# Kernel tuning notes

Hardware: AMD Instinct MI355X
Metric: run time of the kernel (lower is better)

## Reference

```python
import jax, jax.numpy as jnp
import numpy as np

I_DIM, H_DIM, O_DIM = 4, 8, 1


def setup_inputs() -> dict:
    key = jax.random.key(0)
    ks = jax.random.split(key, 7)
    B, T = 8192, 512
    s_ih = 1.0 / np.sqrt(H_DIM)
    x = jax.random.normal(ks[0], (B, T, I_DIM), dtype=jnp.float32)
    # PyTorch LSTM params: gate order i, f, g, o stacked along first axis (4H)
    W_ih = jax.random.uniform(ks[1], (4 * H_DIM, I_DIM), jnp.float32, -s_ih, s_ih)
    W_hh = jax.random.uniform(ks[2], (4 * H_DIM, H_DIM), jnp.float32, -s_ih, s_ih)
    b_ih = jax.random.uniform(ks[3], (4 * H_DIM,), jnp.float32, -s_ih, s_ih)
    b_hh = jax.random.uniform(ks[4], (4 * H_DIM,), jnp.float32, -s_ih, s_ih)
    W_fc = jax.random.uniform(ks[5], (O_DIM, H_DIM), jnp.float32, -s_ih, s_ih)
    b_fc = jax.random.uniform(ks[6], (O_DIM,), jnp.float32, -s_ih, s_ih)
    return {"x": x, "W_ih": W_ih, "W_hh": W_hh, "b_ih": b_ih, "b_hh": b_hh,
            "W_fc": W_fc, "b_fc": b_fc}


def _lstm_last_hidden(x, W_ih, W_hh, b_ih, b_hh):
    B, T, _ = x.shape
    H = W_hh.shape[1]
    # Precompute input projections for all timesteps: [B, T, 4H] -> [T, B, 4H]
    xg = jnp.einsum('bti,gi->btg', x, W_ih) + b_ih + b_hh
    xg = jnp.transpose(xg, (1, 0, 2))
    h0 = jnp.zeros((B, H), x.dtype)
    c0 = jnp.zeros((B, H), x.dtype)

    def step(carry, g_t):
        h, c = carry
        gates = g_t + h @ W_hh.T  # [B, 4H]
        i, f, g, o = jnp.split(gates, 4, axis=-1)
        i = jax.nn.sigmoid(i)
        f = jax.nn.sigmoid(f)
        g = jnp.tanh(g)
        o = jax.nn.sigmoid(o)
        c = f * c + i * g
        h = o * jnp.tanh(c)
        return (h, c), None

    (h_last, _), _ = jax.lax.scan(step, (h0, c0), xg)
    return h_last  # equals out[:, -1, :]


def reference(x, W_ih, W_hh, b_ih, b_hh, W_fc, b_fc):
    h_last = _lstm_last_hidden(x, W_ih, W_hh, b_ih, b_hh)
    return h_last @ W_fc.T + b_fc  # [B, output_dim]
```

## Files before the change

### kernel.cpp

```cpp
#include <hip/hip_runtime.h>

#define T_STEPS 512
#define CHUNK   32
#define NCHUNK  (T_STEPS / CHUNK)
#define EPB     32
#define ROWF    132
#define BUFF    (EPB * ROWF)
#define LOG2E   1.4426950408889634f

typedef float v2f __attribute__((ext_vector_type(2)));

__device__ __forceinline__ v2f pk_fma_b(v2f w, float s, v2f c) {
    v2f sv; sv.x = s;
    v2f d;
    asm("v_pk_fma_f32 %0, %1, %2, %3 op_sel_hi:[1,0,1]"
        : "=v"(d) : "v"(w), "v"(sv), "v"(c));
    return d;
}
__device__ __forceinline__ void pk_fma_acc(v2f& a, v2f w, float s) {
    v2f sv; sv.x = s;
    asm("v_pk_fma_f32 %0, %1, %2, %0 op_sel_hi:[1,0,1]"
        : "+v"(a) : "v"(w), "v"(sv));
}
__device__ __forceinline__ v2f pk_mul_b(v2f w, float s) {
    v2f sv; sv.x = s;
    v2f d;
    asm("v_pk_mul_f32 %0, %1, %2 op_sel_hi:[1,0]"
        : "=v"(d) : "v"(w), "v"(sv));
    return d;
}
__device__ __forceinline__ v2f pk_add2(v2f a, v2f b) {
    v2f d;
    asm("v_pk_add_f32 %0, %1, %2" : "=v"(d) : "v"(a), "v"(b));
    return d;
}

template <int CTRL>
__device__ __forceinline__ float dppf(float v) {
    return __int_as_float(__builtin_amdgcn_update_dpp(
        0, __float_as_int(v), CTRL, 0xF, 0xF, true));
}

__global__ __launch_bounds__(256) void lstm_kernel(
    const float* __restrict__ x, const float* __restrict__ W_ih,
    const float* __restrict__ W_hh, const float* __restrict__ b_ih,
    const float* __restrict__ b_hh, const float* __restrict__ W_fc,
    const float* __restrict__ b_fc, float* __restrict__ out, int B)
{
    __shared__ float ldsx[2 * BUFF];

    const int tid = threadIdx.x;
    const int e   = tid >> 3;
    const int j   = tid & 7;

    const float nL  = -LOG2E;
    const float n2L = -2.0f * LOG2E;
    const float P2L =  2.0f * LOG2E;

    const int ri = j, rf = 8 + j, rg = 16 + j, ro = 24 + j;
    v2f wihIF[4], wihGO[4], whhIF[8], whhGO[8], biasIF, biasGO;
    #pragma unroll
    for (int k = 0; k < 4; ++k) {
        wihIF[k] = v2f{nL  * W_ih[ri * 4 + k], nL * W_ih[rf * 4 + k]};
        wihGO[k] = v2f{n2L * W_ih[rg * 4 + k], nL * W_ih[ro * 4 + k]};
    }
    #pragma unroll
    for (int s = 0; s < 8; ++s) {
        const int m = j ^ s;
        whhIF[s] = v2f{nL  * W_hh[ri * 8 + m], nL * W_hh[rf * 8 + m]};
        whhGO[s] = v2f{n2L * W_hh[rg * 8 + m], nL * W_hh[ro * 8 + m]};
    }
    biasIF = v2f{nL  * (b_ih[ri] + b_hh[ri]), nL * (b_ih[rf] + b_hh[rf])};
    biasGO = v2f{n2L * (b_ih[rg] + b_hh[rg]), nL * (b_ih[ro] + b_hh[ro])};

    const int st  = tid & 31;
    const int se0 = tid >> 5;
    const float* gp0 = x + (size_t)(blockIdx.x * EPB + se0) * (T_STEPS * 4) + st * 4;
    const int wl0 = se0 * ROWF + st * 4;

    float4 v0, v1, v2, v3;
    v0 = *(const float4*)(gp0);
    v1 = *(const float4*)(gp0 + 8 * 2048);
    v2 = *(const float4*)(gp0 + 16 * 2048);
    v3 = *(const float4*)(gp0 + 24 * 2048);
    *(float4*)&ldsx[wl0 + 0 * 8 * ROWF] = v0;
    *(float4*)&ldsx[wl0 + 1 * 8 * ROWF] = v1;
    *(float4*)&ldsx[wl0 + 2 * 8 * ROWF] = v2;
    *(float4*)&ldsx[wl0 + 3 * 8 * ROWF] = v3;
    v0 = *(const float4*)(gp0 + CHUNK * 4);
    v1 = *(const float4*)(gp0 + CHUNK * 4 + 8 * 2048);
    v2 = *(const float4*)(gp0 + CHUNK * 4 + 16 * 2048);
    v3 = *(const float4*)(gp0 + CHUNK * 4 + 24 * 2048);
    __syncthreads();

    float h = 0.0f, ct = 0.0f;

    for (int n = 0; n < NCHUNK; ++n) {
        const int wb = ((n + 1) & 1) * BUFF + wl0;
        *(float4*)&ldsx[wb + 0 * 8 * ROWF] = v0;
        *(float4*)&ldsx[wb + 1 * 8 * ROWF] = v1;
        *(float4*)&ldsx[wb + 2 * 8 * ROWF] = v2;
        *(float4*)&ldsx[wb + 3 * 8 * ROWF] = v3;
        const int t2 = ((n + 2) & (NCHUNK - 1)) * (CHUNK * 4);
        v0 = *(const float4*)(gp0 + t2);
        v1 = *(const float4*)(gp0 + t2 + 8 * 2048);
        v2 = *(const float4*)(gp0 + t2 + 16 * 2048);
        v3 = *(const float4*)(gp0 + t2 + 24 * 2048);

        const float* xr = &ldsx[(n & 1) * BUFF + e * ROWF];
        float4 xc = *(const float4*)(xr);
        #pragma unroll
        for (int t = 0; t < CHUNK; ++t) {
            const float4 xn = *(const float4*)(xr + (((t + 1) & (CHUNK - 1)) * 4));
            const float4 xt = xc;

            v2f xIF = pk_fma_b(wihIF[0], xt.x, biasIF);
            v2f xGO = pk_fma_b(wihGO[0], xt.x, biasGO);
            pk_fma_acc(xIF, wihIF[1], xt.y);  pk_fma_acc(xGO, wihGO[1], xt.y);
            pk_fma_acc(xIF, wihIF[2], xt.z);  pk_fma_acc(xGO, wihGO[2], xt.z);
            pk_fma_acc(xIF, wihIF[3], xt.w);  pk_fma_acc(xGO, wihGO[3], xt.w);

            const float s1 = dppf<0xB1>(h);
            const float s2 = dppf<0x4E>(h);
            const float s3 = dppf<0x1B>(h);
            const float s7 = dppf<0x141>(h);
            const float s4 = dppf<0x1B>(s7);
            const float s5 = dppf<0x4E>(s7);
            const float s6 = dppf<0xB1>(s7);

            v2f aIF = pk_fma_b(whhIF[0], h,  xIF);
            v2f bIF = pk_mul_b(whhIF[1], s1);
            v2f aGO = pk_fma_b(whhGO[0], h,  xGO);
            v2f bGO = pk_mul_b(whhGO[1], s1);
            pk_fma_acc(aIF, whhIF[2], s2);    pk_fma_acc(aGO, whhGO[2], s2);
            pk_fma_acc(bIF, whhIF[3], s3);    pk_fma_acc(bGO, whhGO[3], s3);
            pk_fma_acc(aIF, whhIF[4], s4);    pk_fma_acc(aGO, whhGO[4], s4);
            pk_fma_acc(bIF, whhIF[5], s5);    pk_fma_acc(bGO, whhGO[5], s5);
            pk_fma_acc(aIF, whhIF[6], s6);    pk_fma_acc(aGO, whhGO[6], s6);
            pk_fma_acc(bIF, whhIF[7], s7);    pk_fma_acc(bGO, whhGO[7], s7);
            const v2f gIF = pk_add2(aIF, bIF);
            const v2f gGO = pk_add2(aGO, bGO);

            const float eI = __builtin_amdgcn_exp2f(gIF.x);
            const float eF = __builtin_amdgcn_exp2f(gIF.y);
            const float eG = __builtin_amdgcn_exp2f(gGO.x);
            const float eO = __builtin_amdgcn_exp2f(gGO.y);

            const float R  = __builtin_amdgcn_rcpf((1.0f + eI) * (1.0f + eG));
            const float f_ = __builtin_amdgcn_rcpf(1.0f + eF);
            const float ign = fmaf(eG, P2L, n2L) * R;
            ct = fmaf(f_, ct, ign);
            const float eC = __builtin_amdgcn_exp2f(ct);
            const float RC = __builtin_amdgcn_rcpf((1.0f + eO) * (1.0f + eC));
            h = (1.0f - eC) * RC;

            xc = xn;
        }
        __syncthreads();
    }

    float pr = h * W_fc[j];
    pr += __shfl_xor(pr, 1);
    pr += __shfl_xor(pr, 2);
    pr += __shfl_xor(pr, 4);
    if (j == 0) out[blockIdx.x * EPB + e] = pr + b_fc[0];
}

extern "C" void kernel_launch(void* const* d_in, const int* in_sizes, int n_in,
                              void* d_out, int out_size, void* d_ws, size_t ws_size,
                              hipStream_t stream) {
    const float* x    = (const float*)d_in[0];
    const float* W_ih = (const float*)d_in[1];
    const float* W_hh = (const float*)d_in[2];
    const float* b_ih = (const float*)d_in[3];
    const float* b_hh = (const float*)d_in[4];
    const float* W_fc = (const float*)d_in[5];
    const float* b_fc = (const float*)d_in[6];
    float* out = (float*)d_out;

    const int B = in_sizes[0] / (T_STEPS * 4);
    const int block = 256;
    const int grid = (B * 8) / block;
    lstm_kernel<<<grid, block, 0, stream>>>(x, W_ih, W_hh, b_ih, b_hh, W_fc, b_fc, out, B);
}
```

Baseline: 173.6 us.

## Split each LSTM element across 16 lanes, pairing gate rows per half

Result: slower. 201.5 us (+16.0%).

```diff
diff --git a/kernel.cpp b/kernel.cpp
--- a/kernel.cpp
+++ b/kernel.cpp
@@ -9,27 +9,22 @@
 #define LOG2E   1.4426950408889634f
 
 typedef float v2f __attribute__((ext_vector_type(2)));
+typedef float v4f __attribute__((ext_vector_type(4)));
 
-__device__ __forceinline__ v2f pk_fma_b(v2f w, float s, v2f c) {
-    v2f sv; sv.x = s;
+__device__ __forceinline__ v2f pk_fma2(v2f a, v2f b, v2f c) {
     v2f d;
-    asm("v_pk_fma_f32 %0, %1, %2, %3 op_sel_hi:[1,0,1]"
-        : "=v"(d) : "v"(w), "v"(sv), "v"(c));
+    asm("v_pk_fma_f32 %0, %1, %2, %3" : "=v"(d) : "v"(a), "v"(b), "v"(c));
     return d;
 }
-__device__ __forceinline__ void pk_fma_acc(v2f& a, v2f w, float s) {
-    v2f sv; sv.x = s;
-    asm("v_pk_fma_f32 %0, %1, %2, %0 op_sel_hi:[1,0,1]"
-        : "+v"(a) : "v"(w), "v"(sv));
+__device__ __forceinline__ void pk_fma2_acc(v2f& a, v2f w, v2f s) {
+    asm("v_pk_fma_f32 %0, %1, %2, %0" : "+v"(a) : "v"(w), "v"(s));
 }
-__device__ __forceinline__ v2f pk_mul_b(v2f w, float s) {
-    v2f sv; sv.x = s;
+__device__ __forceinline__ v2f pk_mul2(v2f a, v2f b) {
     v2f d;
-    asm("v_pk_mul_f32 %0, %1, %2 op_sel_hi:[1,0]"
-        : "=v"(d) : "v"(w), "v"(sv));
+    asm("v_pk_mul_f32 %0, %1, %2" : "=v"(d) : "v"(a), "v"(b));
     return d;
 }
-__device__ __forceinline__ v2f pk_add2(v2f a, v2f b) {
+__device__ __forceinline__ v2f pk_add2v(v2f a, v2f b) {
     v2f d;
     asm("v_pk_add_f32 %0, %1, %2" : "=v"(d) : "v"(a), "v"(b));
     return d;
@@ -41,7 +36,7 @@
         0, __float_as_int(v), CTRL, 0xF, 0xF, true));
 }
 
-__global__ __launch_bounds__(256) void lstm_kernel(
+__global__ __launch_bounds__(512) void lstm_kernel(
     const float* __restrict__ x, const float* __restrict__ W_ih,
     const float* __restrict__ W_hh, const float* __restrict__ b_ih,
     const float* __restrict__ b_hh, const float* __restrict__ W_fc,
@@ -50,120 +45,120 @@
     __shared__ float ldsx[2 * BUFF];
 
     const int tid = threadIdx.x;
-    const int e   = tid >> 3;
-    const int j   = tid & 7;
+    const int e   = tid >> 4;
+    const int L   = tid & 15;
+    const int j   = L & 7;
+    const bool hGO = (L & 8) != 0;
 
     const float nL  = -LOG2E;
     const float n2L = -2.0f * LOG2E;
     const float P2L =  2.0f * LOG2E;
 
-    const int ri = j, rf = 8 + j, rg = 16 + j, ro = 24 + j;
-    v2f wihIF[4], wihGO[4], whhIF[8], whhGO[8], biasIF, biasGO;
-    #pragma unroll
-    for (int k = 0; k < 4; ++k) {
-        wihIF[k] = v2f{nL  * W_ih[ri * 4 + k], nL * W_ih[rf * 4 + k]};
-        wihGO[k] = v2f{n2L * W_ih[rg * 4 + k], nL * W_ih[ro * 4 + k]};
-    }
-    #pragma unroll
-    for (int s = 0; s < 8; ++s) {
-        const int m = j ^ s;
-        whhIF[s] = v2f{nL  * W_hh[ri * 8 + m], nL * W_hh[rf * 8 + m]};
-        whhGO[s] = v2f{n2L * W_hh[rg * 8 + m], nL * W_hh[ro * 8 + m]};
-    }
-    biasIF = v2f{nL  * (b_ih[ri] + b_hh[ri]), nL * (b_ih[rf] + b_hh[rf])};
-    biasGO = v2f{n2L * (b_ih[rg] + b_hh[rg]), nL * (b_ih[ro] + b_hh[ro])};
+    const int r0 = hGO ? 16 + j : j;
+    const int r1 = hGO ? 24 + j : 8 + j;
+    const float sc0 = hGO ? n2L : nL;
+    const float sc1 = nL;
+
+    const v2f wx0_0 = v2f{sc0 * W_ih[r0 * 4 + 0], sc0 * W_ih[r0 * 4 + 1]};
+    const v2f wx1_0 = v2f{sc0 * W_ih[r0 * 4 + 2], sc0 * W_ih[r0 * 4 + 3]};
+    const v2f wx0_1 = v2f{sc1 * W_ih[r1 * 4 + 0], sc1 * W_ih[r1 * 4 + 1]};
+    const v2f wx1_1 = v2f{sc1 * W_ih[r1 * 4 + 2], sc1 * W_ih[r1 * 4 + 3]};
+
+    const v2f wh0_0 = v2f{sc0 * W_hh[r0 * 8 + (j ^ 0)], sc0 * W_hh[r0 * 8 + (j ^ 1)]};
+    const v2f wh1_0 = v2f{sc0 * W_hh[r0 * 8 + (j ^ 2)], sc0 * W_hh[r0 * 8 + (j ^ 3)]};
+    const v2f wh2_0 = v2f{sc0 * W_hh[r0 * 8 + (j ^ 4)], sc0 * W_hh[r0 * 8 + (j ^ 5)]};
+    const v2f wh3_0 = v2f{sc0 * W_hh[r0 * 8 + (j ^ 7)], sc0 * W_hh[r0 * 8 + (j ^ 6)]};
+    const v2f wh0_1 = v2f{sc1 * W_hh[r1 * 8 + (j ^ 0)], sc1 * W_hh[r1 * 8 + (j ^ 1)]};
+    const v2f wh1_1 = v2f{sc1 * W_hh[r1 * 8 + (j ^ 2)], sc1 * W_hh[r1 * 8 + (j ^ 3)]};
+    const v2f wh2_1 = v2f{sc1 * W_hh[r1 * 8 + (j ^ 4)], sc1 * W_hh[r1 * 8 + (j ^ 5)]};
+    const v2f wh3_1 = v2f{sc1 * W_hh[r1 * 8 + (j ^ 7)], sc1 * W_hh[r1 * 8 + (j ^ 6)]};
+
+    const v2f bias0 = v2f{sc0 * (b_ih[r0] + b_hh[r0]), 0.0f};
+    const v2f bias1 = v2f{sc1 * (b_ih[r1] + b_hh[r1]), 0.0f};
 
     const int st  = tid & 31;
     const int se0 = tid >> 5;
     const float* gp0 = x + (size_t)(blockIdx.x * EPB + se0) * (T_STEPS * 4) + st * 4;
     const int wl0 = se0 * ROWF + st * 4;
 
-    float4 v0, v1, v2, v3;
-    v0 = *(const float4*)(gp0);
-    v1 = *(const float4*)(gp0 + 8 * 2048);
-    v2 = *(const float4*)(gp0 + 16 * 2048);
-    v3 = *(const float4*)(gp0 + 24 * 2048);
-    *(float4*)&ldsx[wl0 + 0 * 8 * ROWF] = v0;
-    *(float4*)&ldsx[wl0 + 1 * 8 * ROWF] = v1;
-    *(float4*)&ldsx[wl0 + 2 * 8 * ROWF] = v2;
-    *(float4*)&ldsx[wl0 + 3 * 8 * ROWF] = v3;
-    v0 = *(const float4*)(gp0 + CHUNK * 4);
-    v1 = *(const float4*)(gp0 + CHUNK * 4 + 8 * 2048);
-    v2 = *(const float4*)(gp0 + CHUNK * 4 + 16 * 2048);
-    v3 = *(const float4*)(gp0 + CHUNK * 4 + 24 * 2048);
+    v4f v0, v1;
+    v0 = *(const v4f*)(gp0);
+    v1 = *(const v4f*)(gp0 + 16 * 2048);
+    *(v4f*)&ldsx[wl0 + 0 * 16 * ROWF] = v0;
+    *(v4f*)&ldsx[wl0 + 1 * 16 * ROWF] = v1;
+    v0 = *(const v4f*)(gp0 + CHUNK * 4);
+    v1 = *(const v4f*)(gp0 + CHUNK * 4 + 16 * 2048);
     __syncthreads();
 
-    float h = 0.0f, ct = 0.0f;
+    v2f hv = v2f{0.0f, 0.0f};
+    float ct = 0.0f;
 
     for (int n = 0; n < NCHUNK; ++n) {
         const int wb = ((n + 1) & 1) * BUFF + wl0;
-        *(float4*)&ldsx[wb + 0 * 8 * ROWF] = v0;
-        *(float4*)&ldsx[wb + 1 * 8 * ROWF] = v1;
-        *(float4*)&ldsx[wb + 2 * 8 * ROWF] = v2;
-        *(float4*)&ldsx[wb + 3 * 8 * ROWF] = v3;
+        *(v4f*)&ldsx[wb + 0 * 16 * ROWF] = v0;
+        *(v4f*)&ldsx[wb + 1 * 16 * ROWF] = v1;
         const int t2 = ((n + 2) & (NCHUNK - 1)) * (CHUNK * 4);
-        v0 = *(const float4*)(gp0 + t2);
-        v1 = *(const float4*)(gp0 + t2 + 8 * 2048);
-        v2 = *(const float4*)(gp0 + t2 + 16 * 2048);
-        v3 = *(const float4*)(gp0 + t2 + 24 * 2048);
+        v0 = *(const v4f*)(gp0 + t2);
+        v1 = *(const v4f*)(gp0 + t2 + 16 * 2048);
 
         const float* xr = &ldsx[(n & 1) * BUFF + e * ROWF];
-        float4 xc = *(const float4*)(xr);
+        v4f xc = *(const v4f*)(xr);
         #pragma unroll
         for (int t = 0; t < CHUNK; ++t) {
-            const float4 xn = *(const float4*)(xr + (((t + 1) & (CHUNK - 1)) * 4));
-            const float4 xt = xc;
+            const v4f xn = *(const v4f*)(xr + (((t + 1) & (CHUNK - 1)) * 4));
+            const v4f xt = xc;
+            const v2f x01 = __builtin_shufflevector(xt, xt, 0, 1);
+            const v2f x23 = __builtin_shufflevector(xt, xt, 2, 3);
 
-            v2f xIF = pk_fma_b(wihIF[0], xt.x, biasIF);
-            v2f xGO = pk_fma_b(wihGO[0], xt.x, biasGO);
-            pk_fma_acc(xIF, wihIF[1], xt.y);  pk_fma_acc(xGO, wihGO[1], xt.y);
-            pk_fma_acc(xIF, wihIF[2], xt.z);  pk_fma_acc(xGO, wihGO[2], xt.z);
-            pk_fma_acc(xIF, wihIF[3], xt.w);  pk_fma_acc(xGO, wihGO[3], xt.w);
+            v2f A0 = pk_fma2(wx0_0, x01, bias0);
+            v2f A1 = pk_fma2(wx0_1, x01, bias1);
+            v2f B0 = pk_mul2(wx1_0, x23);
+            v2f B1 = pk_mul2(wx1_1, x23);
 
-            const float s1 = dppf<0xB1>(h);
-            const float s2 = dppf<0x4E>(h);
-            const float s3 = dppf<0x1B>(h);
-            const float s7 = dppf<0x141>(h);
-            const float s4 = dppf<0x1B>(s7);
-            const float s5 = dppf<0x4E>(s7);
-            const float s6 = dppf<0xB1>(s7);
+            hv.y = dppf<0xB1>(hv.x);
+            v2f p1p; p1p.x = dppf<0x4E>(hv.x);
+                     p1p.y = dppf<0x1B>(hv.x);
+            v2f p3p; p3p.x = dppf<0x141>(hv.x);
+                     p3p.y = dppf<0xB1>(p3p.x);
+            v2f p2p; p2p.x = dppf<0x1B>(p3p.x);
+                     p2p.y = dppf<0x4E>(p3p.x);
 
-            v2f aIF = pk_fma_b(whhIF[0], h,  xIF);
-            v2f bIF = pk_mul_b(whhIF[1], s1);
-            v2f aGO = pk_fma_b(whhGO[0], h,  xGO);
-            v2f bGO = pk_mul_b(whhGO[1], s1);
-            pk_fma_acc(aIF, whhIF[2], s2);    pk_fma_acc(aGO, whhGO[2], s2);
-            pk_fma_acc(bIF, whhIF[3], s3);    pk_fma_acc(bGO, whhGO[3], s3);
-            pk_fma_acc(aIF, whhIF[4], s4);    pk_fma_acc(aGO, whhGO[4], s4);
-            pk_fma_acc(bIF, whhIF[5], s5);    pk_fma_acc(bGO, whhGO[5], s5);
-            pk_fma_acc(aIF, whhIF[6], s6);    pk_fma_acc(aGO, whhGO[6], s6);
-            pk_fma_acc(bIF, whhIF[7], s7);    pk_fma_acc(bGO, whhGO[7], s7);
-            const v2f gIF = pk_add2(aIF, bIF);
-            const v2f gGO = pk_add2(aGO, bGO);
+            pk_fma2_acc(A0, wh0_0, hv);   pk_fma2_acc(A1, wh0_1, hv);
+            pk_fma2_acc(B0, wh1_0, p1p);  pk_fma2_acc(B1, wh1_1, p1p);
+            pk_fma2_acc(A0, wh2_0, p2p);  pk_fma2_acc(A1, wh2_1, p2p);
+            pk_fma2_acc(B0, wh3_0, p3p);  pk_fma2_acc(B1, wh3_1, p3p);
+            const v2f S0 = pk_add2v(A0, B0);
+            const v2f S1 = pk_add2v(A1, B1);
+            const float g0 = S0.x + S0.y;
+            const float g1 = S1.x + S1.y;
 
-            const float eI = __builtin_amdgcn_exp2f(gIF.x);
-            const float eF = __builtin_amdgcn_exp2f(gIF.y);
-            const float eG = __builtin_amdgcn_exp2f(gGO.x);
-            const float eO = __builtin_amdgcn_exp2f(gGO.y);
+            const float eA  = __builtin_amdgcn_exp2f(g0);
+            const float eB  = __builtin_amdgcn_exp2f(g1);
+            const float eA8 = dppf<0x140>(dppf<0x141>(eA));
+            const float eB8 = dppf<0x140>(dppf<0x141>(eB));
 
-            const float R  = __builtin_amdgcn_rcpf((1.0f + eI) * (1.0f + eG));
-            const float f_ = __builtin_amdgcn_rcpf(1.0f + eF);
-            const float ign = fmaf(eG, P2L, n2L) * R;
+            const float eGv = hGO ? eA  : eA8;
+            const float eFv = hGO ? eB8 : eB;
+            const float eOv = hGO ? eB  : eB8;
+
+            const float R   = __builtin_amdgcn_rcpf((1.0f + eA) * (1.0f + eA8));
+            const float f_  = __builtin_amdgcn_rcpf(1.0f + eFv);
+            const float ign = fmaf(eGv, P2L, n2L) * R;
             ct = fmaf(f_, ct, ign);
             const float eC = __builtin_amdgcn_exp2f(ct);
-            const float RC = __builtin_amdgcn_rcpf((1.0f + eO) * (1.0f + eC));
-            h = (1.0f - eC) * RC;
+            const float RC = __builtin_amdgcn_rcpf((1.0f + eOv) * (1.0f + eC));
+            hv.x = (1.0f - eC) * RC;
 
             xc = xn;
         }
         __syncthreads();
     }
 
-    float pr = h * W_fc[j];
+    float pr = hv.x * W_fc[j];
     pr += __shfl_xor(pr, 1);
     pr += __shfl_xor(pr, 2);
     pr += __shfl_xor(pr, 4);
-    if (j == 0) out[blockIdx.x * EPB + e] = pr + b_fc[0];
+    if (L == 0) out[blockIdx.x * EPB + e] = pr + b_fc[0];
 }
 
 extern "C" void kernel_launch(void* const* d_in, const int* in_sizes, int n_in,
@@ -179,7 +174,7 @@
     float* out = (float*)d_out;
 
     const int B = in_sizes[0] / (T_STEPS * 4);
-    const int block = 256;
-    const int grid = (B * 8) / block;
+    const int block = 512;
+    const int grid = B / EPB;
     lstm_kernel<<<grid, block, 0, stream>>>(x, W_ih, W_hh, b_ih, b_hh, W_fc, b_fc, out, B);
 }
```
